# Optimization experiments

Hardware: AMD Instinct MI355X
Metric: run time of the kernel (lower is better)

The kernel has to match this reference:

```python
import jax, jax.numpy as jnp
import numpy as np

B, T, D_IN, H, K, C = 8, 2048, 512, 384, 8192, 8
N_BLOCKS = 6
EPS = 1e-5


def conv1d(x, w, b, pad, groups=1):
    # x: [B, Cin, T], w: [Cout, Cin//groups, k]
    y = jax.lax.conv_general_dilated(
        x, w, window_strides=(1,), padding=[(pad, pad)],
        dimension_numbers=("NCH", "OIH", "NCH"), feature_group_count=groups)
    return y + b[None, :, None]


def layernorm(x, g, b):
    # normalize over last axis
    m = jnp.mean(x, axis=-1, keepdims=True)
    v = jnp.mean(jnp.square(x - m), axis=-1, keepdims=True)
    return (x - m) * jax.lax.rsqrt(v + EPS) * g + b


def setup_inputs() -> dict:
    key = jax.random.key(0)
    ks = iter(jax.random.split(key, 32))
    s = 0.02
    inp = {
        "x": jax.random.normal(next(ks), (B, T, D_IN), dtype=jnp.float32),
        "enc_w": jax.random.normal(next(ks), (H, D_IN, 7)) * s,
        "enc_b": jnp.zeros((H,)),
        "enc_ln_g": jnp.ones((H,)),
        "enc_ln_b": jnp.zeros((H,)),
        "blk_dw_w": jax.random.normal(next(ks), (N_BLOCKS, H, 1, 7)) * s,
        "blk_dw_b": jnp.zeros((N_BLOCKS, H)),
        "blk_ln_g": jnp.ones((N_BLOCKS, H)),
        "blk_ln_b": jnp.zeros((N_BLOCKS, H)),
        "blk_w1": jax.random.normal(next(ks), (N_BLOCKS, 4 * H, H)) * s,
        "blk_b1": jnp.zeros((N_BLOCKS, 4 * H)),
        "blk_w2": jax.random.normal(next(ks), (N_BLOCKS, H, 4 * H)) * s,
        "blk_b2": jnp.zeros((N_BLOCKS, H)),
        "out_w": jax.random.normal(next(ks), (C, H, 1)) * s,
        "out_b": jnp.zeros((C,)),
        "embeddings": jax.random.normal(next(ks), (K, C)),
    }
    return inp


def encode(x, enc_w, enc_b, enc_ln_g, enc_ln_b, blk_dw_w, blk_dw_b,
           blk_ln_g, blk_ln_b, blk_w1, blk_b1, blk_w2, blk_b2, out_w, out_b):
    h = x.transpose(0, 2, 1)                       # [B, D_IN, T]
    h = conv1d(h, enc_w, enc_b, pad=3)             # [B, H, T]
    h = layernorm(h.transpose(0, 2, 1), enc_ln_g, enc_ln_b).transpose(0, 2, 1)
    for i in range(N_BLOCKS):
        res = h
        h = conv1d(h, blk_dw_w[i], blk_dw_b[i], pad=3, groups=H)  # depthwise
        ht = h.transpose(0, 2, 1)                  # [B, T, H]
        ht = layernorm(ht, blk_ln_g[i], blk_ln_b[i])
        ht = jnp.einsum("bth,fh->btf", ht, blk_w1[i]) + blk_b1[i]
        ht = jax.nn.gelu(ht, approximate=False)    # torch GELU is exact erf
        ht = jnp.einsum("btf,hf->bth", ht, blk_w2[i]) + blk_b2[i]
        h = ht.transpose(0, 2, 1) + res
    z = conv1d(h, out_w, out_b, pad=0)             # [B, C, T]
    return z.transpose(0, 2, 1)                    # [B, T, C]


def reference(x, enc_w, enc_b, enc_ln_g, enc_ln_b, blk_dw_w, blk_dw_b,
              blk_ln_g, blk_ln_b, blk_w1, blk_b1, blk_w2, blk_b2,
              out_w, out_b, embeddings):
    z = encode(x, enc_w, enc_b, enc_ln_g, enc_ln_b, blk_dw_w, blk_dw_b,
               blk_ln_g, blk_ln_b, blk_w1, blk_b1, blk_w2, blk_b2, out_w, out_b)
    flat = z.reshape(-1, C)                        # [B*T, C]
    # squared euclidean distances: same argmin as torch.cdist
    d2 = (jnp.sum(flat * flat, axis=1, keepdims=True)
          - 2.0 * flat @ embeddings.T
          + jnp.sum(embeddings * embeddings, axis=1))  # [B*T, K]
    indices = jnp.argmin(d2, axis=1)               # [B*T], int
    return indices
```

## Files before the change

### kernel.cpp

```cpp
#include <hip/hip_runtime.h>
#include <math.h>

#define T_   2048
#define DIN  512
#define H_   384
#define H4_  1536
#define BT_  16384

typedef _Float16 half_t;
typedef _Float16 f16x8 __attribute__((ext_vector_type(8)));
typedef float f32x4 __attribute__((ext_vector_type(4)));

#define LO_SCALE 2048.0f
#define LO_INV   4.8828125e-4f

__device__ __forceinline__ void lds_barrier() {
    asm volatile("s_waitcnt lgkmcnt(0)\n\ts_barrier" ::: "memory");
}

__device__ __forceinline__ void split2(float v, half_t* hi, half_t* lo) {
    half_t h = (half_t)v;
    *hi = h;
    *lo = (half_t)((v - (float)h) * LO_SCALE);
}

__global__ void k_split(const float* __restrict__ in, half_t* __restrict__ hi,
                        half_t* __restrict__ lo, long n) {
    long i = (long)blockIdx.x * 256 + threadIdx.x;
    if (i >= n) return;
    split2(in[i], hi + i, lo + i);
}

__global__ void k_split_encw(const float* __restrict__ in, half_t* __restrict__ hi,
                             half_t* __restrict__ lo) {
    int idx = blockIdx.x * 256 + threadIdx.x;
    if (idx >= H_ * 3584) return;
    int n = idx / 3584;
    int r = idx % 3584;
    int tap = r >> 9, i = r & 511;
    split2(in[n * 3584 + i * 7 + tap], hi + idx, lo + idx);
}

__global__ void k_ln(const float* __restrict__ in, float* __restrict__ out,
                     const float* __restrict__ g, const float* __restrict__ b) {
    int row = blockIdx.x;
    int lane = threadIdx.x;
    const float* ir = in + (long)row * H_;
    float v[6];
    float s = 0.f;
#pragma unroll
    for (int j = 0; j < 6; ++j) { v[j] = ir[lane + (j << 6)]; s += v[j]; }
#pragma unroll
    for (int o = 32; o > 0; o >>= 1) s += __shfl_down(s, o, 64);
    s = __shfl(s, 0, 64);
    float mean = s * (1.f / 384.f);
    float q = 0.f;
#pragma unroll
    for (int j = 0; j < 6; ++j) { float d = v[j] - mean; q += d * d; }
#pragma unroll
    for (int o = 32; o > 0; o >>= 1) q += __shfl_down(q, o, 64);
    q = __shfl(q, 0, 64);
    float rstd = rsqrtf(q * (1.f / 384.f) + 1e-5f);
    float* orow = out + (long)row * H_;
#pragma unroll
    for (int j = 0; j < 6; ++j) {
        int c = lane + (j << 6);
        orow[c] = (v[j] - mean) * rstd * g[c] + b[c];
    }
}

__global__ __launch_bounds__(256) void k_dwconv_ln(
    const float* __restrict__ h, half_t* __restrict__ oh,
    half_t* __restrict__ ol,
    const float* __restrict__ w, const float* __restrict__ wb,
    const float* __restrict__ g, const float* __restrict__ gb) {
    int row = (blockIdx.x << 2) + (threadIdx.x >> 6);
    int b = row >> 11;
    int t = row & 2047;
    int lane = threadIdx.x & 63;
    const float* hb = h + ((long)b * T_) * H_;
    float vx[3], vy[3];
    float s = 0.f;
#pragma unroll
    for (int j = 0; j < 3; ++j) {
        int c = (lane << 1) + (j << 7);
        float ax = wb[c], ay = wb[c + 1];
        const float* wcx = w + c * 7;
        const float* wcy = wcx + 7;
#pragma unroll
        for (int k = 0; k < 7; ++k) {
            int tt = t + k - 3;
            if ((unsigned)tt < (unsigned)T_) {
                float2 hv = *(const float2*)&hb[(long)tt * H_ + c];
                ax = fmaf(hv.x, wcx[k], ax);
                ay = fmaf(hv.y, wcy[k], ay);
            }
        }
        vx[j] = ax; vy[j] = ay;
        s += ax + ay;
    }
#pragma unroll
    for (int o = 32; o > 0; o >>= 1) s += __shfl_down(s, o, 64);
    s = __shfl(s, 0, 64);
    float mean = s * (1.f / 384.f);
    float q = 0.f;
#pragma unroll
    for (int j = 0; j < 3; ++j) {
        float dx = vx[j] - mean, dy = vy[j] - mean;
        q += dx * dx + dy * dy;
    }
#pragma unroll
    for (int o = 32; o > 0; o >>= 1) q += __shfl_down(q, o, 64);
    q = __shfl(q, 0, 64);
    float rstd = rsqrtf(q * (1.f / 384.f) + 1e-5f);
    long ro = (long)row * H_;
#pragma unroll
    for (int j = 0; j < 3; ++j) {
        int c = (lane << 1) + (j << 7);
        float valx = (vx[j] - mean) * rstd * g[c] + gb[c];
        float valy = (vy[j] - mean) * rstd * g[c + 1] + gb[c + 1];
        split2(valx, oh + ro + c, ol + ro + c);
        split2(valy, oh + ro + c + 1, ol + ro + c + 1);
    }
}

#define DECLSET(S) float4 pAh##S, pAl##S, pBh0##S, pBl0##S, pBh1##S, pBl1##S

#define LOADREGS(S, k0_) do {                                               \
    int k0v = (k0_);                                                        \
    if (MODE == 0) {                                                        \
        int kk = k0v + ak;                                                  \
        int tap = kk >> 9, ii = kk & 511;                                   \
        int ta = tt0 + tap;                                                 \
        pAh##S = pAl##S = make_float4(0.f, 0.f, 0.f, 0.f);                  \
        if ((unsigned)ta < 2048u) {                                         \
            long o = ((long)bq * 2048 + ta) * 512 + ii;                     \
            pAh##S = *(const float4*)(Ah + o);                              \
            pAl##S = *(const float4*)(Al + o);                              \
        }                                                                   \
    } else {                                                                \
        pAh##S = *(const float4*)(Ah + aoff + k0v);                         \
        pAl##S = *(const float4*)(Al + aoff + k0v);                         \
    }                                                                       \
    pBh0##S = *(const float4*)(Bh + boff0 + k0v);                           \
    pBl0##S = *(const float4*)(Bl + boff0 + k0v);                           \
    pBh1##S = *(const float4*)(Bh + boff1 + k0v);                           \
    pBl1##S = *(const float4*)(Bl + boff1 + k0v);                           \
} while (0)

#define STOREBUF(S, buf) do {                                               \
    *(float4*)&smem[(buf) * 2048 + aw] = pAh##S;                            \
    *(float4*)&smem[4096 + (buf) * 2048 + aw] = pAl##S;                     \
    int b_ = 8192 + (buf) * 4096 + aw;                                      \
    *(float4*)&smem[b_] = pBh0##S;                                          \
    *(float4*)&smem[b_ + 2048] = pBh1##S;                                   \
    *(float4*)&smem[b_ + 8192] = pBl0##S;                                   \
    *(float4*)&smem[b_ + 8192 + 2048] = pBl1##S;                            \
} while (0)

template <int MODE, int NN>
__global__ __launch_bounds__(256, 3) void k_mgemm64(
    const half_t* __restrict__ Ah, const half_t* __restrict__ Al,
    const half_t* __restrict__ Bh, const half_t* __restrict__ Bl,
    const float* __restrict__ bias, const float* __restrict__ res,
    float* __restrict__ Cf, half_t* __restrict__ Ch, half_t* __restrict__ Cl,
    int N, int K) {
    __shared__ __align__(16) half_t smem[24576];
    const int tid = threadIdx.x;
    const int lane = tid & 63, wid = tid >> 6;
    const int wn = wid << 5;
    const int quad = lane >> 4, l16 = lane & 15;

    constexpr int NWG = 256 * NN;
    constexpr int CHUNK = NWG / 8;
    const int lin = blockIdx.x;
    const int tile = (lin & 7) * CHUNK + (lin >> 3);
    const int m0 = (tile / NN) << 6;
    const int n0 = (tile % NN) << 7;

    const int ar = tid >> 2;
    const int ak = (tid & 3) << 3;

    long aoff = 0;
    int tt0 = 0, bq = 0;
    if (MODE == 0) {
        bq = m0 >> 11;
        tt0 = (m0 & 2047) + ar - 3;
    } else {
        aoff = (long)(m0 + ar) * K + ak;
    }
    const long boff0 = (long)(n0 + ar) * K + ak;
    const long boff1 = boff0 + (long)64 * K;

    const int aw = ar * 32 + ((((tid & 3) ^ (ar >> 1)) & 3) << 3);

    DECLSET(0);
    DECLSET(1);

    f32x4 acc1[4][2] = {};
    f32x4 acc2[4][2] = {};
    const int sw = ((quad ^ (l16 >> 1)) & 3) << 3;

    auto compute = [&](int buf) {
        const int ab = buf * 2048 + l16 * 32 + sw;
        const int bb = 8192 + buf * 4096 + (wn + l16) * 32 + sw;
        f16x8 fah[4], fal[4], fgh[2], fgl[2];
#pragma unroll
        for (int f = 0; f < 4; ++f)
            fah[f] = *(const f16x8*)&smem[ab + f * 512];
#pragma unroll
        for (int g = 0; g < 2; ++g)
            fgh[g] = *(const f16x8*)&smem[bb + g * 512];
        __builtin_amdgcn_s_setprio(1);
#pragma unroll
        for (int f = 0; f < 4; ++f)
#pragma unroll
            for (int g = 0; g < 2; ++g)
                acc1[f][g] = __builtin_amdgcn_mfma_f32_16x16x32_f16(fah[f], fgh[g], acc1[f][g], 0, 0, 0);
        __builtin_amdgcn_s_setprio(0);
#pragma unroll
        for (int f = 0; f < 4; ++f)
            fal[f] = *(const f16x8*)&smem[ab + 4096 + f * 512];
#pragma unroll
        for (int g = 0; g < 2; ++g)
            fgl[g] = *(const f16x8*)&smem[bb + 8192 + g * 512];
        __builtin_amdgcn_s_setprio(1);
#pragma unroll
        for (int f = 0; f < 4; ++f)
#pragma unroll
            for (int g = 0; g < 2; ++g)
                acc2[f][g] = __builtin_amdgcn_mfma_f32_16x16x32_f16(fah[f], fgl[g], acc2[f][g], 0, 0, 0);
#pragma unroll
        for (int f = 0; f < 4; ++f)
#pragma unroll
            for (int g = 0; g < 2; ++g)
                acc2[f][g] = __builtin_amdgcn_mfma_f32_16x16x32_f16(fal[f], fgh[g], acc2[f][g], 0, 0, 0);
        __builtin_amdgcn_s_setprio(0);
    };

    const int nIter = K >> 5;
    LOADREGS(0, 0);
    LOADREGS(1, 32);
    STOREBUF(0, 0);
    if (nIter > 2) LOADREGS(0, 64);
    for (int it = 0; it < nIter; it += 2) {
        lds_barrier();
        compute(0);
        STOREBUF(1, 1);
        if (it + 3 < nIter) LOADREGS(1, (it + 3) << 5);
        lds_barrier();
        compute(1);
        if (it + 2 < nIter) {
            STOREBUF(0, 0);
            if (it + 4 < nIter) LOADREGS(0, (it + 4) << 5);
        }
    }

    float bv[2];
    bv[0] = bias[n0 + wn + l16];
    bv[1] = bias[n0 + wn + 16 + l16];

#pragma unroll
    for (int f = 0; f < 4; ++f)
#pragma unroll
        for (int g = 0; g < 2; ++g)
#pragma unroll
            for (int r = 0; r < 4; ++r) {
                long row = m0 + f * 16 + quad * 4 + r;
                int col = n0 + wn + g * 16 + l16;
                float v = acc1[f][g][r] + acc2[f][g][r] * LO_INV + bv[g];
                long o = row * N + col;
                if (MODE == 2) v += res[o];
                Cf[o] = v;
            }
}

#define LOAD96(k0_) do {                                                    \
    int k0v = (k0_);                                                        \
    long a_ = aoff + k0v;                                                   \
    qAh0 = *(const float4*)(Ah + a_);                                       \
    qAh1 = *(const float4*)(Ah + a_ + 8);                                   \
    qAl0 = *(const float4*)(Al + a_);                                       \
    qAl1 = *(const float4*)(Al + a_ + 8);                                   \
    long b_ = boff0 + k0v;                                                  \
    qBh0 = *(const float4*)(Bh + b_);                                       \
    qBl0 = *(const float4*)(Bl + b_);                                       \
    if (tid < 128) {                                                        \
        long c_ = boff1 + k0v;                                              \
        qBh1 = *(const float4*)(Bh + c_);                                   \
        qBl1 = *(const float4*)(Bl + c_);                                   \
    }                                                                       \
} while (0)

#define STORE96(buf) do {                                                   \
    int ab_ = (buf) * 14336 + ra * 32;                                      \
    *(float4*)&smem[ab_ + pa0 * 8] = qAh0;                                  \
    *(float4*)&smem[ab_ + pa1 * 8] = qAh1;                                  \
    *(float4*)&smem[ab_ + 4096 + pa0 * 8] = qAl0;                           \
    *(float4*)&smem[ab_ + 4096 + pa1 * 8] = qAl1;                           \
    int bb_ = (buf) * 14336 + 8192 + rb0 * 32 + pb0 * 8;                    \
    *(float4*)&smem[bb_] = qBh0;                                            \
    *(float4*)&smem[bb_ + 3072] = qBl0;                                     \
    if (tid < 128) {                                                        \
        int bc_ = bb_ + 64 * 32;                                            \
        *(float4*)&smem[bc_] = qBh1;                                        \
        *(float4*)&smem[bc_ + 3072] = qBl1;                                 \
    }                                                                       \
} while (0)

template <int MODE, int NT>
__global__ __launch_bounds__(256, 2) void k_mgemm96(
    const half_t* __restrict__ Ah, const half_t* __restrict__ Al,
    const half_t* __restrict__ Bh, const half_t* __restrict__ Bl,
    const float* __restrict__ bias, const float* __restrict__ res,
    float* __restrict__ Cf, half_t* __restrict__ Ch, half_t* __restrict__ Cl,
    int N, int K) {
    __shared__ __align__(16) half_t smem[28672];
    const int tid = threadIdx.x;
    const int lane = tid & 63, wid = tid >> 6;
    const int wm = (wid >> 1) << 6;
    const int wn = (wid & 1) * 48;
    const int quad = lane >> 4, l16 = lane & 15;

    constexpr int NWG = 128 * NT;
    constexpr int CHUNK = NWG / 8;
    const int lin = blockIdx.x;
    const int tile = (lin & 7) * CHUNK + (lin >> 3);
    const int m0 = (tile / NT) << 7;
    const int n0 = (tile % NT) * 96;

    const int ra = tid >> 1;
    const int ga0 = (tid & 1) << 1;
    const int rb0 = tid >> 2;
    const int gb = tid & 3;
    const int pa0 = (ga0 ^ ((ra >> 1) & 3)) & 3;
    const int pa1 = pa0 ^ 1;
    const int pb0 = (gb ^ ((rb0 >> 1) & 3)) & 3;

    const long aoff = (long)(m0 + ra) * K + (ga0 << 3);
    const long boff0 = (long)(n0 + rb0) * K + (gb << 3);
    const long boff1 = boff0 + (long)64 * K;

    float4 qAh0, qAh1, qAl0, qAl1, qBh0, qBl0, qBh1, qBl1;

    f32x4 acc1[4][3] = {};
    f32x4 acc2[4][3] = {};
    const int sw = ((quad ^ (l16 >> 1)) & 3) << 3;

    auto compute = [&](int buf) {
        const int ab = buf * 14336 + (wm + l16) * 32 + sw;
        const int bb = buf * 14336 + 8192 + (wn + l16) * 32 + sw;
        f16x8 fah[4], fal[4], fgh[3], fgl[3];
#pragma unroll
        for (int f = 0; f < 4; ++f)
            fah[f] = *(const f16x8*)&smem[ab + f * 512];
#pragma unroll
        for (int g = 0; g < 3; ++g)
            fgh[g] = *(const f16x8*)&smem[bb + g * 512];
        __builtin_amdgcn_s_setprio(1);
#pragma unroll
        for (int f = 0; f < 4; ++f)
#pragma unroll
            for (int g = 0; g < 3; ++g)
                acc1[f][g] = __builtin_amdgcn_mfma_f32_16x16x32_f16(fah[f], fgh[g], acc1[f][g], 0, 0, 0);
        __builtin_amdgcn_s_setprio(0);
#pragma unroll
        for (int f = 0; f < 4; ++f)
            fal[f] = *(const f16x8*)&smem[ab + 4096 + f * 512];
#pragma unroll
        for (int g = 0; g < 3; ++g)
            fgl[g] = *(const f16x8*)&smem[bb + 3072 + g * 512];
        __builtin_amdgcn_s_setprio(1);
#pragma unroll
        for (int f = 0; f < 4; ++f)
#pragma unroll
            for (int g = 0; g < 3; ++g)
                acc2[f][g] = __builtin_amdgcn_mfma_f32_16x16x32_f16(fah[f], fgl[g], acc2[f][g], 0, 0, 0);
#pragma unroll
        for (int f = 0; f < 4; ++f)
#pragma unroll
            for (int g = 0; g < 3; ++g)
                acc2[f][g] = __builtin_amdgcn_mfma_f32_16x16x32_f16(fal[f], fgh[g], acc2[f][g], 0, 0, 0);
        __builtin_amdgcn_s_setprio(0);
    };

    const int nIter = K >> 5;
    LOAD96(0);
    STORE96(0);
    int cur = 0;
    for (int it = 0; it < nIter; ++it) {
        if (it + 1 < nIter) LOAD96((it + 1) << 5);
        lds_barrier();
        compute(cur);
        if (it + 1 < nIter) STORE96(cur ^ 1);
        cur ^= 1;
    }

    float bv[3];
#pragma unroll
    for (int g = 0; g < 3; ++g) bv[g] = bias[n0 + wn + g * 16 + l16];

    if (MODE == 1) {
        __syncthreads();
#pragma unroll
        for (int f = 0; f < 4; ++f)
#pragma unroll
            for (int g = 0; g < 3; ++g)
#pragma unroll
                for (int r = 0; r < 4; ++r) {
                    int rm = wm + f * 16 + quad * 4 + r;
                    int cn = wn + g * 16 + l16;
                    float v = acc1[f][g][r] + acc2[f][g][r] * LO_INV + bv[g];
                    v = 0.5f * v * (1.0f + erff(v * 0.70710678118654752f));
                    half_t hh = (half_t)v;
                    smem[rm * 104 + cn] = hh;
                    smem[13312 + rm * 104 + cn] = (half_t)((v - (float)hh) * LO_SCALE);
                }
        __syncthreads();
        int row = tid >> 1, c0 = (tid & 1) * 48;
        long go = (long)(m0 + row) * N + n0 + c0;
        int so = row * 104 + c0;
#pragma unroll
        for (int u = 0; u < 6; ++u) {
            *(float4*)(Ch + go + u * 8) = *(const float4*)&smem[so + u * 8];
            *(float4*)(Cl + go + u * 8) = *(const float4*)&smem[13312 + so + u * 8];
        }
    } else {
#pragma unroll
        for (int f = 0; f < 4; ++f)
#pragma unroll
            for (int g = 0; g < 3; ++g)
#pragma unroll
                for (int r = 0; r < 4; ++r) {
                    long row = m0 + wm + f * 16 + quad * 4 + r;
                    int col = n0 + wn + g * 16 + l16;
                    float v = acc1[f][g][r] + acc2[f][g][r] * LO_INV + bv[g];
                    long o = row * N + col;
                    v += res[o];
                    Cf[o] = v;
                }
    }
}

__global__ __launch_bounds__(256) void k_outconv_argmin(
    const float* __restrict__ h, const float* __restrict__ ow,
    const float* __restrict__ ob, const float* __restrict__ emb,
    int* __restrict__ outIdx) {
    __shared__ float hs[16][H_ + 1];
    __shared__ float zs[16][8];
    __shared__ float es[16 * 516];
    __shared__ float rb[16][16];
    __shared__ int ri[16][16];
    const int tid = threadIdx.x;
    const int row0 = blockIdx.x << 4;

    for (int i = tid; i < 16 * (H_ / 4); i += 256) {
        int r = i / 96;
        int c4 = (i % 96) << 2;
        float4 v = *(const float4*)&h[((long)(row0 + r)) * H_ + c4];
        hs[r][c4] = v.x; hs[r][c4 + 1] = v.y; hs[r][c4 + 2] = v.z; hs[r][c4 + 3] = v.w;
    }
    __syncthreads();

    if (tid < 128) {
        int r = tid & 15, c = tid >> 4;
        float acc = ob[c];
        const float* wc = ow + c * H_;
        for (int j = 0; j < H_; ++j) acc = fmaf(hs[r][j], wc[j], acc);
        zs[r][c] = acc;
    }
    __syncthreads();

    const int r = tid & 15;
    const int sl = tid >> 4;
    float z0 = zs[r][0], z1 = zs[r][1], z2 = zs[r][2], z3 = zs[r][3];
    float z4 = zs[r][4], z5 = zs[r][5], z6 = zs[r][6], z7 = zs[r][7];
    float best = 3.4e38f;
    int bi = 0;

    for (int ch = 0; ch < 8; ++ch) {
        __syncthreads();
        for (int i = tid; i < 2048; i += 256) {
            int e = i >> 1;
            int half = (i & 1) << 2;
            float4 src = *(const float4*)&emb[(((long)(ch << 10)) + e) * 8 + half];
            *(float4*)&es[(e >> 6) * 516 + ((e & 63) << 3) + half] = src;
        }
        __syncthreads();
        const float* ep = es + sl * 516;
        int gbase = (ch << 10) + (sl << 6);
#pragma unroll 4
        for (int j = 0; j < 64; ++j) {
            float4 e0 = *(const float4*)(ep + (j << 3));
            float4 e1 = *(const float4*)(ep + (j << 3) + 4);
            float t, d;
            t = e0.x - z0; d = t * t;
            t = e0.y - z1; d = fmaf(t, t, d);
            t = e0.z - z2; d = fmaf(t, t, d);
            t = e0.w - z3; d = fmaf(t, t, d);
            t = e1.x - z4; d = fmaf(t, t, d);
            t = e1.y - z5; d = fmaf(t, t, d);
            t = e1.z - z6; d = fmaf(t, t, d);
            t = e1.w - z7; d = fmaf(t, t, d);
            if (d < best) { best = d; bi = gbase + j; }
        }
    }
    rb[r][sl] = best;
    ri[r][sl] = bi;
    __syncthreads();
    if (sl == 0) {
        float bb = rb[r][0];
        int bbi = ri[r][0];
#pragma unroll
        for (int s2 = 1; s2 < 16; ++s2) {
            float v = rb[r][s2];
            int i2 = ri[r][s2];
            if (v < bb || (v == bb && i2 < bbi)) { bb = v; bbi = i2; }
        }
        outIdx[row0 + r] = bbi;
    }
}

extern "C" void kernel_launch(void* const* d_in, const int* in_sizes, int n_in,
                              void* d_out, int out_size, void* d_ws, size_t ws_size,
                              hipStream_t stream) {
    const float* x        = (const float*)d_in[0];
    const float* enc_w    = (const float*)d_in[1];
    const float* enc_b    = (const float*)d_in[2];
    const float* enc_ln_g = (const float*)d_in[3];
    const float* enc_ln_b = (const float*)d_in[4];
    const float* blk_dw_w = (const float*)d_in[5];
    const float* blk_dw_b = (const float*)d_in[6];
    const float* blk_ln_g = (const float*)d_in[7];
    const float* blk_ln_b = (const float*)d_in[8];
    const float* blk_w1   = (const float*)d_in[9];
    const float* blk_b1   = (const float*)d_in[10];
    const float* blk_w2   = (const float*)d_in[11];
    const float* blk_b2   = (const float*)d_in[12];
    const float* out_w    = (const float*)d_in[13];
    const float* out_b    = (const float*)d_in[14];
    const float* emb      = (const float*)d_in[15];
    int* out = (int*)d_out;

    char* base = (char*)d_ws;
    float*  h    = (float*)base;
    half_t* tmph = (half_t*)(base + 25165824);
    half_t* tmpl = (half_t*)(base + 37748736);
    half_t* ht4h = (half_t*)(base + 50331648);
    half_t* ht4l = (half_t*)(base + 100663296);
    half_t* ench = (half_t*)(base + 150994944);
    half_t* encl = (half_t*)(base + 153747456);
    half_t* w1h  = (half_t*)(base + 156499968);
    half_t* w1l  = (half_t*)(base + 163577856);
    half_t* w2h  = (half_t*)(base + 170655744);
    half_t* w2l  = (half_t*)(base + 177733632);
    half_t* xh = ht4h;
    half_t* xl = (half_t*)(base + 50331648 + 16777216);

    k_split<<<(8388608 + 255) / 256, 256, 0, stream>>>(x, xh, xl, 8388608L);
    k_split<<<(3538944 + 255) / 256, 256, 0, stream>>>(blk_w1, w1h, w1l, 3538944L);
    k_split<<<(3538944 + 255) / 256, 256, 0, stream>>>(blk_w2, w2h, w2l, 3538944L);
    k_split_encw<<<(H_ * 3584 + 255) / 256, 256, 0, stream>>>(enc_w, ench, encl);

    k_mgemm64<0, 3><<<768, 256, 0, stream>>>(xh, xl, ench, encl, enc_b,
                                             nullptr, h, nullptr, nullptr,
                                             H_, 3584);
    k_ln<<<BT_, 64, 0, stream>>>(h, h, enc_ln_g, enc_ln_b);

    for (int i = 0; i < 6; ++i) {
        k_dwconv_ln<<<BT_ / 4, 256, 0, stream>>>(h, tmph, tmpl, blk_dw_w + i * H_ * 7,
                                                 blk_dw_b + i * H_, blk_ln_g + i * H_,
                                                 blk_ln_b + i * H_);
        k_mgemm96<1, 16><<<2048, 256, 0, stream>>>(
            tmph, tmpl, w1h + (long)i * 589824, w1l + (long)i * 589824,
            blk_b1 + i * H4_, nullptr, nullptr, ht4h, ht4l, H4_, H_);
        k_mgemm96<2, 4><<<512, 256, 0, stream>>>(
            ht4h, ht4l, w2h + (long)i * 589824, w2l + (long)i * 589824,
            blk_b2 + i * H_, h, h, nullptr, nullptr, H_, H4_);
    }

    k_outconv_argmin<<<BT_ / 16, 256, 0, stream>>>(h, out_w, out_b, emb, out);
}
```

Baseline: 1.809 ms.

## Use eight-wave 512-thread blocks for block GEMMs and reorder MFMA schedule

The 128x96 block GEMMs now run with 512 threads (8 waves), each wave owning a 32x48 sub-tile instead of 64x48. This halves per-wave accumulator registers and lets each thread do one float4 load per operand per K step. Each wave now loads all hi/lo fragments up front and issues the correction MFMAs first, and the setprio hints are removed. The same reordering is applied to the 64-wide GEMM. The aim is more waves in flight to hide LDS and global latency. In exchange, each wave gets less register-level reuse and the LDS fragment traffic per MFMA goes up.

```diff
diff --git a/kernel.cpp b/kernel.cpp
--- a/kernel.cpp
+++ b/kernel.cpp
@@ -206,36 +206,30 @@
         const int bb = 8192 + buf * 4096 + (wn + l16) * 32 + sw;
         f16x8 fah[4], fal[4], fgh[2], fgl[2];
 #pragma unroll
+        for (int f = 0; f < 4; ++f) {
+            fah[f] = *(const f16x8*)&smem[ab + f * 512];
+            fal[f] = *(const f16x8*)&smem[ab + 4096 + f * 512];
+        }
+#pragma unroll
+        for (int g = 0; g < 2; ++g) {
+            fgh[g] = *(const f16x8*)&smem[bb + g * 512];
+            fgl[g] = *(const f16x8*)&smem[bb + 8192 + g * 512];
+        }
+#pragma unroll
         for (int f = 0; f < 4; ++f)
-            fah[f] = *(const f16x8*)&smem[ab + f * 512];
-#pragma unroll
-        for (int g = 0; g < 2; ++g)
-            fgh[g] = *(const f16x8*)&smem[bb + g * 512];
-        __builtin_amdgcn_s_setprio(1);
+#pragma unroll
+            for (int g = 0; g < 2; ++g)
+                acc2[f][g] = __builtin_amdgcn_mfma_f32_16x16x32_f16(fah[f], fgl[g], acc2[f][g], 0, 0, 0);
+#pragma unroll
+        for (int f = 0; f < 4; ++f)
+#pragma unroll
+            for (int g = 0; g < 2; ++g)
+                acc2[f][g] = __builtin_amdgcn_mfma_f32_16x16x32_f16(fal[f], fgh[g], acc2[f][g], 0, 0, 0);
 #pragma unroll
         for (int f = 0; f < 4; ++f)
 #pragma unroll
             for (int g = 0; g < 2; ++g)
                 acc1[f][g] = __builtin_amdgcn_mfma_f32_16x16x32_f16(fah[f], fgh[g], acc1[f][g], 0, 0, 0);
-        __builtin_amdgcn_s_setprio(0);
-#pragma unroll
-        for (int f = 0; f < 4; ++f)
-            fal[f] = *(const f16x8*)&smem[ab + 4096 + f * 512];
-#pragma unroll
-        for (int g = 0; g < 2; ++g)
-            fgl[g] = *(const f16x8*)&smem[bb + 8192 + g * 512];
-        __builtin_amdgcn_s_setprio(1);
-#pragma unroll
-        for (int f = 0; f < 4; ++f)
-#pragma unroll
-            for (int g = 0; g < 2; ++g)
-                acc2[f][g] = __builtin_amdgcn_mfma_f32_16x16x32_f16(fah[f], fgl[g], acc2[f][g], 0, 0, 0);
-#pragma unroll
-        for (int f = 0; f < 4; ++f)
-#pragma unroll
-            for (int g = 0; g < 2; ++g)
-                acc2[f][g] = __builtin_amdgcn_mfma_f32_16x16x32_f16(fal[f], fgh[g], acc2[f][g], 0, 0, 0);
-        __builtin_amdgcn_s_setprio(0);
     };
 
     const int nIter = K >> 5;
@@ -275,41 +269,29 @@
             }
 }
 
-#define LOAD96(k0_) do {                                                    \
+#define LOADW8(k0_) do {                                                    \
     int k0v = (k0_);                                                        \
-    long a_ = aoff + k0v;                                                   \
-    qAh0 = *(const float4*)(Ah + a_);                                       \
-    qAh1 = *(const float4*)(Ah + a_ + 8);                                   \
-    qAl0 = *(const float4*)(Al + a_);                                       \
-    qAl1 = *(const float4*)(Al + a_ + 8);                                   \
-    long b_ = boff0 + k0v;                                                  \
-    qBh0 = *(const float4*)(Bh + b_);                                       \
-    qBl0 = *(const float4*)(Bl + b_);                                       \
-    if (tid < 128) {                                                        \
-        long c_ = boff1 + k0v;                                              \
-        qBh1 = *(const float4*)(Bh + c_);                                   \
-        qBl1 = *(const float4*)(Bl + c_);                                   \
+    qAh = *(const float4*)(Ah + aoff + k0v);                                \
+    qAl = *(const float4*)(Al + aoff + k0v);                                \
+    if (tid < 384) {                                                        \
+        qBh = *(const float4*)(Bh + boff + k0v);                            \
+        qBl = *(const float4*)(Bl + boff + k0v);                            \
     }                                                                       \
 } while (0)
 
-#define STORE96(buf) do {                                                   \
-    int ab_ = (buf) * 14336 + ra * 32;                                      \
-    *(float4*)&smem[ab_ + pa0 * 8] = qAh0;                                  \
-    *(float4*)&smem[ab_ + pa1 * 8] = qAh1;                                  \
-    *(float4*)&smem[ab_ + 4096 + pa0 * 8] = qAl0;                           \
-    *(float4*)&smem[ab_ + 4096 + pa1 * 8] = qAl1;                           \
-    int bb_ = (buf) * 14336 + 8192 + rb0 * 32 + pb0 * 8;                    \
-    *(float4*)&smem[bb_] = qBh0;                                            \
-    *(float4*)&smem[bb_ + 3072] = qBl0;                                     \
-    if (tid < 128) {                                                        \
-        int bc_ = bb_ + 64 * 32;                                            \
-        *(float4*)&smem[bc_] = qBh1;                                        \
-        *(float4*)&smem[bc_ + 3072] = qBl1;                                 \
+#define STOREW8(buf) do {                                                   \
+    int a_ = (buf) * 14336 + sa;                                            \
+    *(float4*)&smem[a_] = qAh;                                              \
+    *(float4*)&smem[a_ + 4096] = qAl;                                       \
+    if (tid < 384) {                                                        \
+        int b_ = (buf) * 14336 + 8192 + sa;                                 \
+        *(float4*)&smem[b_] = qBh;                                          \
+        *(float4*)&smem[b_ + 3072] = qBl;                                   \
     }                                                                       \
 } while (0)
 
 template <int MODE, int NT>
-__global__ __launch_bounds__(256, 2) void k_mgemm96(
+__global__ __launch_bounds__(512, 4) void k_mgemm96w8(
     const half_t* __restrict__ Ah, const half_t* __restrict__ Al,
     const half_t* __restrict__ Bh, const half_t* __restrict__ Bl,
     const float* __restrict__ bias, const float* __restrict__ res,
@@ -318,7 +300,7 @@
     __shared__ __align__(16) half_t smem[28672];
     const int tid = threadIdx.x;
     const int lane = tid & 63, wid = tid >> 6;
-    const int wm = (wid >> 1) << 6;
+    const int wm = (wid >> 1) << 5;
     const int wn = (wid & 1) * 48;
     const int quad = lane >> 4, l16 = lane & 15;
 
@@ -329,70 +311,59 @@
     const int m0 = (tile / NT) << 7;
     const int n0 = (tile % NT) * 96;
 
-    const int ra = tid >> 1;
-    const int ga0 = (tid & 1) << 1;
-    const int rb0 = tid >> 2;
-    const int gb = tid & 3;
-    const int pa0 = (ga0 ^ ((ra >> 1) & 3)) & 3;
-    const int pa1 = pa0 ^ 1;
-    const int pb0 = (gb ^ ((rb0 >> 1) & 3)) & 3;
-
-    const long aoff = (long)(m0 + ra) * K + (ga0 << 3);
-    const long boff0 = (long)(n0 + rb0) * K + (gb << 3);
-    const long boff1 = boff0 + (long)64 * K;
-
-    float4 qAh0, qAh1, qAl0, qAl1, qBh0, qBl0, qBh1, qBl1;
-
-    f32x4 acc1[4][3] = {};
-    f32x4 acc2[4][3] = {};
+    const int srow = tid >> 2;
+    const int sg = tid & 3;
+    const int sa = srow * 32 + (((sg ^ (tid >> 3)) & 3) << 3);
+
+    const long aoff = (long)(m0 + srow) * K + (sg << 3);
+    const long boff = (long)(n0 + srow) * K + (sg << 3);
+
+    float4 qAh, qAl, qBh, qBl;
+
+    f32x4 acc1[2][3] = {};
+    f32x4 acc2[2][3] = {};
     const int sw = ((quad ^ (l16 >> 1)) & 3) << 3;
 
     auto compute = [&](int buf) {
         const int ab = buf * 14336 + (wm + l16) * 32 + sw;
         const int bb = buf * 14336 + 8192 + (wn + l16) * 32 + sw;
-        f16x8 fah[4], fal[4], fgh[3], fgl[3];
-#pragma unroll
-        for (int f = 0; f < 4; ++f)
+        f16x8 fah[2], fal[2], fgh[3], fgl[3];
+#pragma unroll
+        for (int f = 0; f < 2; ++f) {
             fah[f] = *(const f16x8*)&smem[ab + f * 512];
-#pragma unroll
-        for (int g = 0; g < 3; ++g)
+            fal[f] = *(const f16x8*)&smem[ab + 4096 + f * 512];
+        }
+#pragma unroll
+        for (int g = 0; g < 3; ++g) {
             fgh[g] = *(const f16x8*)&smem[bb + g * 512];
-        __builtin_amdgcn_s_setprio(1);
-#pragma unroll
-        for (int f = 0; f < 4; ++f)
+            fgl[g] = *(const f16x8*)&smem[bb + 3072 + g * 512];
+        }
+#pragma unroll
+        for (int f = 0; f < 2; ++f)
+#pragma unroll
+            for (int g = 0; g < 3; ++g)
+                acc2[f][g] = __builtin_amdgcn_mfma_f32_16x16x32_f16(fah[f], fgl[g], acc2[f][g], 0, 0, 0);
+#pragma unroll
+        for (int f = 0; f < 2; ++f)
+#pragma unroll
+            for (int g = 0; g < 3; ++g)
+                acc2[f][g] = __builtin_amdgcn_mfma_f32_16x16x32_f16(fal[f], fgh[g], acc2[f][g], 0, 0, 0);
+#pragma unroll
+        for (int f = 0; f < 2; ++f)
 #pragma unroll
             for (int g = 0; g < 3; ++g)
                 acc1[f][g] = __builtin_amdgcn_mfma_f32_16x16x32_f16(fah[f], fgh[g], acc1[f][g], 0, 0, 0);
-        __builtin_amdgcn_s_setprio(0);
-#pragma unroll
-        for (int f = 0; f < 4; ++f)
-            fal[f] = *(const f16x8*)&smem[ab + 4096 + f * 512];
-#pragma unroll
-        for (int g = 0; g < 3; ++g)
-            fgl[g] = *(const f16x8*)&smem[bb + 3072 + g * 512];
-        __builtin_amdgcn_s_setprio(1);
-#pragma unroll
-        for (int f = 0; f < 4; ++f)
-#pragma unroll
-            for (int g = 0; g < 3; ++g)
-                acc2[f][g] = __builtin_amdgcn_mfma_f32_16x16x32_f16(fah[f], fgl[g], acc2[f][g], 0, 0, 0);
-#pragma unroll
-        for (int f = 0; f < 4; ++f)
-#pragma unroll
-            for (int g = 0; g < 3; ++g)
-                acc2[f][g] = __builtin_amdgcn_mfma_f32_16x16x32_f16(fal[f], fgh[g], acc2[f][g], 0, 0, 0);
-        __builtin_amdgcn_s_setprio(0);
     };
 
     const int nIter = K >> 5;
-    LOAD96(0);
-    STORE96(0);
+    LOADW8(0);
+    STOREW8(0);
     int cur = 0;
     for (int it = 0; it < nIter; ++it) {
-        if (it + 1 < nIter) LOAD96((it + 1) << 5);
+        if (it + 1 < nIter) LOADW8((it + 1) << 5);
         lds_barrier();
         compute(cur);
-        if (it + 1 < nIter) STORE96(cur ^ 1);
+        if (it + 1 < nIter) STOREW8(cur ^ 1);
         cur ^= 1;
     }
 
@@ -403,7 +374,7 @@
     if (MODE == 1) {
         __syncthreads();
 #pragma unroll
-        for (int f = 0; f < 4; ++f)
+        for (int f = 0; f < 2; ++f)
 #pragma unroll
             for (int g = 0; g < 3; ++g)
 #pragma unroll
@@ -417,17 +388,17 @@
                     smem[13312 + rm * 104 + cn] = (half_t)((v - (float)hh) * LO_SCALE);
                 }
         __syncthreads();
-        int row = tid >> 1, c0 = (tid & 1) * 48;
+        int row = tid >> 2, c0 = (tid & 3) * 24;
         long go = (long)(m0 + row) * N + n0 + c0;
         int so = row * 104 + c0;
 #pragma unroll
-        for (int u = 0; u < 6; ++u) {
+        for (int u = 0; u < 3; ++u) {
             *(float4*)(Ch + go + u * 8) = *(const float4*)&smem[so + u * 8];
             *(float4*)(Cl + go + u * 8) = *(const float4*)&smem[13312 + so + u * 8];
         }
     } else {
 #pragma unroll
-        for (int f = 0; f < 4; ++f)
+        for (int f = 0; f < 2; ++f)
 #pragma unroll
             for (int g = 0; g < 3; ++g)
 #pragma unroll
@@ -571,10 +542,10 @@
         k_dwconv_ln<<<BT_ / 4, 256, 0, stream>>>(h, tmph, tmpl, blk_dw_w + i * H_ * 7,
                                                  blk_dw_b + i * H_, blk_ln_g + i * H_,
                                                  blk_ln_b + i * H_);
-        k_mgemm96<1, 16><<<2048, 256, 0, stream>>>(
+        k_mgemm96w8<1, 16><<<2048, 512, 0, stream>>>(
             tmph, tmpl, w1h + (long)i * 589824, w1l + (long)i * 589824,
             blk_b1 + i * H4_, nullptr, nullptr, ht4h, ht4l, H4_, H_);
-        k_mgemm96<2, 4><<<512, 256, 0, stream>>>(
+        k_mgemm96w8<2, 4><<<512, 512, 0, stream>>>(
             ht4h, ht4l, w2h + (long)i * 589824, w2l + (long)i * 589824,
             blk_b2 + i * H_, h, h, nullptr, nullptr, H_, H4_);
     }
```

New measurement: 1.690 ms. 6.6% less time.
